# Kernel optimization log

Hardware: AMD Instinct MI355X
Metric: run time of the kernel (lower is better)

Reference implementation:

```python
import jax, jax.numpy as jnp
import numpy as np

QDEPTH = 20
WIDTH = HEIGHT = 28
PIXELS = WIDTH * HEIGHT          # 784
WIRES = 10                        # ceil(log2(784))
BATCH = 8192


def setup_inputs() -> dict:
    key = jax.random.key(0)
    k1, k2, k3, k4 = jax.random.split(key, 4)
    x = jax.random.normal(k1, (BATCH, 1, WIDTH, HEIGHT), jnp.float32)
    W = jax.random.normal(k2, (WIRES, PIXELS), jnp.float32) / np.sqrt(PIXELS)
    b = jax.random.normal(k3, (WIRES,), jnp.float32) * 0.01
    qweights = jax.random.normal(k4, (QDEPTH, WIRES, 3), jnp.float32) * 0.4
    return {"x": x, "W": W, "b": b, "qweights": qweights}


def _apply_1q(state, gate, wire):
    """Apply a single-qubit gate. state: (B,)+(2,)*WIRES; gate: (2,2) or (B,2,2)."""
    ax = 1 + wire
    s = jnp.moveaxis(state, ax, 1)
    shp = s.shape
    s = s.reshape(shp[0], 2, -1)
    if gate.ndim == 2:
        s = jnp.einsum('ij,bjr->bir', gate, s)
    else:
        s = jnp.einsum('bij,bjr->bir', gate, s)
    return jnp.moveaxis(s.reshape(shp), 1, ax)


def _cnot(state, c, t):
    """CNOT with control c, target t on state (B,)+(2,)*WIRES."""
    s = jnp.moveaxis(state, (1 + c, 1 + t), (1, 2))
    # when control==1, flip target axis
    s = jnp.concatenate([s[:, :1], jnp.flip(s[:, 1:2], axis=2)], axis=1)
    return jnp.moveaxis(s, (1, 2), (1 + c, 1 + t))


def _ry_batched(theta):
    """theta: (B,) -> (B,2,2) complex RY gates."""
    c = jnp.cos(theta / 2)
    s = jnp.sin(theta / 2)
    g = jnp.stack([jnp.stack([c, -s], -1), jnp.stack([s, c], -1)], -2)
    return g.astype(jnp.complex64)


def _rot(phi, theta, omega):
    """PennyLane Rot(phi,theta,omega) = RZ(omega) RY(theta) RZ(phi), scalars -> (2,2)."""
    c = jnp.cos(theta / 2)
    s = jnp.sin(theta / 2)
    m00 = jnp.exp(-0.5j * (phi + omega)) * c
    m01 = -jnp.exp(0.5j * (phi - omega)) * s
    m10 = jnp.exp(-0.5j * (phi - omega)) * s
    m11 = jnp.exp(0.5j * (phi + omega)) * c
    return jnp.stack([jnp.stack([m00, m01]), jnp.stack([m10, m11])]).astype(jnp.complex64)


def _forward(x, W, b, qweights):
    B = x.shape[0]
    feat = x.reshape(B, -1)                       # b 1 w h -> b (w h)
    angles = feat @ W.T + b                       # linear_down -> (B, WIRES)

    # |0...0> statevector, wire 0 most significant (PennyLane convention)
    state = jnp.zeros((B,) + (2,) * WIRES, jnp.complex64)
    state = state.at[(slice(None),) + (0,) * WIRES].set(1.0)

    # AngleEmbedding, rotation='Y'
    for w in range(WIRES):
        state = _apply_1q(state, _ry_batched(angles[:, w]), w)

    # StronglyEntanglingLayers: per-layer Rot on every wire, then CNOT ring
    for l in range(QDEPTH):
        for w in range(WIRES):
            state = _apply_1q(state, _rot(qweights[l, w, 0], qweights[l, w, 1], qweights[l, w, 2]), w)
        r = (l % (WIRES - 1)) + 1                 # default PennyLane ranges
        for w in range(WIRES):
            state = _cnot(state, w, (w + r) % WIRES)

    sv = state.reshape(B, -1)
    probs = sv.real ** 2 + sv.imag ** 2           # qml.probs over all wires
    out = jnp.clip(probs[:, :PIXELS] * PIXELS, 0.0, 1.0)
    return out.reshape(B, 1, WIDTH, HEIGHT)


def reference(x, W, b, qweights):
    return _forward(x, W, b, qweights)
```

## Files before the change

### kernel.cpp

```cpp
#include <hip/hip_runtime.h>
#include <hip/hip_bf16.h>
#include <stdint.h>


#define NWIRES  10
#define DIM     1024
#define NLAYERS 20
#define NGATES  200
#define NPASS   100
#define PIXELS  784
#define BATCH   8192

typedef _Float16 f16;
typedef _Float16 f16x8 __attribute__((ext_vector_type(8)));
typedef float    f32x4 __attribute__((ext_vector_type(4)));
typedef float    f32x2 __attribute__((ext_vector_type(2)));

typedef const __attribute__((address_space(1))) void* gas1_t;
typedef __attribute__((address_space(3))) void*       las3_t;

__device__ __forceinline__ void gload_lds16(const void* g, void* l) {
  __builtin_amdgcn_global_load_lds((gas1_t)g, (las3_t)l, 16, 0, 0);
}

__global__ __launch_bounds__(256) void k_prep(const float* __restrict__ qw,
                                              float* __restrict__ plan_mat,
                                              unsigned* __restrict__ plan_idx,
                                              unsigned* __restrict__ plan_final) {
  __shared__ float gm[NGATES][8];
  const int tid = threadIdx.x;

  if (tid < NGATES) {
    float phi = qw[tid * 3 + 0], th = qw[tid * 3 + 1], om = qw[tid * 3 + 2];
    float s, c, sa, ca, sb, cb;
    sincosf(0.5f * th, &s, &c);
    sincosf(0.5f * (phi + om), &sa, &ca);
    sincosf(0.5f * (phi - om), &sb, &cb);
    gm[tid][0] = ca * c;  gm[tid][1] = sa * c;
    gm[tid][2] = cb * s;  gm[tid][3] = sb * s;
    gm[tid][4] = -cb * s; gm[tid][5] = sb * s;
    gm[tid][6] = ca * c;  gm[tid][7] = -sa * c;
  }
  __syncthreads();

  if (tid == 0) {
    unsigned rowA[NWIRES], invc[NWIRES];
    for (int i = 0; i < NWIRES; i++) { rowA[i] = 1u << i; invc[i] = 1u << i; }
    for (int lrev = 0; lrev < NLAYERS; lrev++) {
      int l = NLAYERS - 1 - lrev;
      int r = (l % (NWIRES - 1)) + 1;
      for (int w = NWIRES - 1; w >= 0; w--) {
        int c = w, t = (w + r) % NWIRES;
        int pc = 9 - c, pt = 9 - t;
        rowA[pt] ^= rowA[pc];
        invc[pc] ^= invc[pt];
      }
      for (int s = 0; s < 5; s++) {
        int w1 = 2 * s, w2 = 2 * s + 1;
        int p1 = 9 - w1, p2 = 9 - w2;
        unsigned u1 = rowA[p1], u2 = rowA[p2];
        unsigned m1 = invc[p1], m2 = invc[p2];
        unsigned b1 = u1 & (0u - u1);
        if (u2 & b1) u2 ^= u1;
        unsigned b2 = u2 & (0u - u2);
        if (u1 & b2) u1 ^= u2;
        unsigned bLo = (b1 < b2) ? b1 : b2;
        unsigned bHi = (b1 < b2) ? b2 : b1;
        unsigned* P = plan_idx + (size_t)(lrev * 5 + s) * 8;
        P[0] = bLo; P[1] = bHi; P[2] = u1; P[3] = u2;
        P[4] = b1;  P[5] = b2;  P[6] = m1; P[7] = m2;
      }
    }
    for (int p = 0; p < NWIRES; p++) plan_final[p] = invc[p];
  } else if (tid >= 100 && tid < 200) {
    int t = tid - 100;
    int lrev = t / 5, s = t % 5;
    int l = NLAYERS - 1 - lrev;
    int g1 = l * NWIRES + 2 * s, g2 = g1 + 1;
    float* K = plan_mat + (size_t)t * 64;
#pragma unroll
    for (int r = 0; r < 4; r++) {
#pragma unroll
      for (int c = 0; c < 4; c++) {
        int r1 = r >> 1, c1 = c >> 1, r2 = r & 1, c2 = c & 1;
        float ar = gm[g1][(r1 * 2 + c1) * 2], ai = gm[g1][(r1 * 2 + c1) * 2 + 1];
        float br = gm[g2][(r2 * 2 + c2) * 2], bi = gm[g2][(r2 * 2 + c2) * 2 + 1];
        float kr = ar * br - ai * bi;
        float ki = ar * bi + ai * br;
        float* e = K + (r * 4 + c) * 4;
        e[0] = kr; e[1] = kr; e[2] = -ki; e[3] = ki;
      }
    }
  }
}

__global__ __launch_bounds__(256) void k_main(const float* __restrict__ plan_mat,
                                              const unsigned* __restrict__ plan_idx,
                                              const unsigned* __restrict__ plan_final,
                                              const float* __restrict__ x,
                                              const float* __restrict__ W,
                                              const float* __restrict__ bias,
                                              f16* __restrict__ E,
                                              f16* __restrict__ Bt) {
  __shared__ f32x2 st[DIM];
  __shared__ float part[4][NWIRES];
  __shared__ float csh[NWIRES][2];

  const int tid = threadIdx.x;

  if (blockIdx.x < PIXELS) {
    const int col = blockIdx.x;

    for (int i = tid; i < DIM; i += 256)
      st[i] = (f32x2){i == col ? 1.f : 0.f, 0.f};
    __syncthreads();

    for (int t = 0; t < NPASS; t++) {
      const unsigned* P = plan_idx + (size_t)t * 8;
      const unsigned bLo = P[0], bHi = P[1], u1 = P[2], u2 = P[3];
      const unsigned pb1 = P[4], pb2 = P[5], m1 = P[6], m2 = P[7];
      const f32x4* Kp = (const f32x4*)(plan_mat + (size_t)t * 64);

      unsigned q  = (unsigned)tid;
      unsigned xx = ((q & ~(bLo - 1u)) << 1) | (q & (bLo - 1u));
      unsigned j0 = ((xx & ~(bHi - 1u)) << 1) | (xx & (bHi - 1u));
      unsigned j  = j0 ^ ((__popc(u1 & j0) & 1) ? pb1 : 0u)
                       ^ ((__popc(u2 & j0) & 1) ? pb2 : 0u);

      f32x2 v0 = st[j];
      f32x2 v1 = st[j ^ m2];
      f32x2 v2 = st[j ^ m1];
      f32x2 v3 = st[j ^ m1 ^ m2];
      f32x2 w0 = {v0.y, v0.x}, w1 = {v1.y, v1.x};
      f32x2 w2 = {v2.y, v2.x}, w3 = {v3.y, v3.x};

      f32x2 r0 = {0.f, 0.f}, r1 = {0.f, 0.f}, r2 = {0.f, 0.f}, r3 = {0.f, 0.f};
#define CM(rr, e, vv, ww)                         \
      { f32x4 kk = Kp[e];                         \
        rr += (f32x2){kk.x, kk.y} * (vv);         \
        rr += (f32x2){kk.z, kk.w} * (ww); }
      CM(r0, 0, v0, w0)  CM(r0, 1, v1, w1)  CM(r0, 2, v2, w2)  CM(r0, 3, v3, w3)
      CM(r1, 4, v0, w0)  CM(r1, 5, v1, w1)  CM(r1, 6, v2, w2)  CM(r1, 7, v3, w3)
      CM(r2, 8, v0, w0)  CM(r2, 9, v1, w1)  CM(r2, 10, v2, w2) CM(r2, 11, v3, w3)
      CM(r3, 12, v0, w0) CM(r3, 13, v1, w1) CM(r3, 14, v2, w2) CM(r3, 15, v3, w3)
#undef CM

      st[j]           = r0;
      st[j ^ m2]      = r1;
      st[j ^ m1]      = r2;
      st[j ^ m1 ^ m2] = r3;
      __syncthreads();
    }

    unsigned invl[NWIRES];
#pragma unroll
    for (int p = 0; p < NWIRES; p++) invl[p] = plan_final[p];

    __align__(8) f16 re4[4], im4[4];
#pragma unroll
    for (int u = 0; u < 4; u++) {
      int i = tid * 4 + u;
      unsigned j = 0;
#pragma unroll
      for (int p = 0; p < NWIRES; p++)
        if ((i >> p) & 1) j ^= invl[p];
      f32x2 v = st[j];
      re4[u] = (f16)v.x;
      im4[u] = (f16)(-v.y);
    }
    *(uint2*)(&Bt[(size_t)(2 * col) * DIM + tid * 4])     = *(const uint2*)re4;
    *(uint2*)(&Bt[(size_t)(2 * col + 1) * DIM + tid * 4]) = *(const uint2*)im4;
    return;
  }

  const int b = blockIdx.x - PIXELS;
  const float* xr = x + (size_t)b * PIXELS;

  float acc[NWIRES];
#pragma unroll
  for (int w = 0; w < NWIRES; w++) acc[w] = 0.f;

  for (int k = tid; k < PIXELS; k += 256) {
    float xv = xr[k];
#pragma unroll
    for (int w = 0; w < NWIRES; w++) acc[w] = fmaf(xv, W[w * PIXELS + k], acc[w]);
  }

#pragma unroll
  for (int w = 0; w < NWIRES; w++) {
    float v = acc[w];
#pragma unroll
    for (int off = 32; off > 0; off >>= 1) v += __shfl_xor(v, off, 64);
    acc[w] = v;
  }

  const int wv = tid >> 6, ln = tid & 63;
  if (ln == 0) {
#pragma unroll
    for (int w = 0; w < NWIRES; w++) part[wv][w] = acc[w];
  }
  __syncthreads();
  if (tid < NWIRES) {
    float a = part[0][tid] + part[1][tid] + part[2][tid] + part[3][tid] + bias[tid];
    float s, c;
    sincosf(0.5f * a, &s, &c);
    csh[tid][0] = c;
    csh[tid][1] = s;
  }
  __syncthreads();

  __align__(8) f16 e4[4];
#pragma unroll
  for (int u = 0; u < 4; u++) {
    int i = tid * 4 + u;
    float pr = 1.f;
#pragma unroll
    for (int w = 0; w < NWIRES; w++) pr *= csh[w][(i >> (9 - w)) & 1];
    e4[u] = (f16)pr;
  }
  *(uint2*)(&E[(size_t)b * DIM + tid * 4]) = *(const uint2*)e4;
}

__device__ __forceinline__ void g_stage(const f16* __restrict__ g, f16* l,
                                        int tid, int row0, int kt) {
#pragma unroll
  for (int r = 0; r < 4; r++) {
    int u = r * 512 + tid;
    int row = u >> 3, c8 = u & 7;
    gload_lds16((const char*)g + (size_t)(row0 + row) * 2048 + kt * 128 + c8 * 16,
                (char*)l + (size_t)u * 16);
  }
}

__global__ __launch_bounds__(512, 2) void k_gemm(const f16* __restrict__ E,
                                                 const f16* __restrict__ Bt,
                                                 float* __restrict__ out) {
  __shared__ __align__(16) f16 As[2][256 * 64];
  __shared__ __align__(16) f16 Bs[2][256 * 64];

  const int tid = threadIdx.x;
  const int wid = tid >> 6, ln = tid & 63;
  const int wm = wid >> 2, wn = wid & 3;

  const int bid = blockIdx.x;
  const int swz = (bid & 7) * 28 + (bid >> 3);
  const int mt  = swz % 32, nt = swz / 32;
  const int m0  = mt * 256;
  const int n0  = nt * 256;

  f32x4 acc[8][4];
#pragma unroll
  for (int a = 0; a < 8; a++)
#pragma unroll
    for (int q = 0; q < 4; q++) acc[a][q] = (f32x4){0.f, 0.f, 0.f, 0.f};

#define COMPUTE(buf)                                                            \
  {                                                                             \
    _Pragma("unroll")                                                           \
    for (int kk = 0; kk < 2; kk++) {                                            \
      f16x8 af[8], bf[4];                                                       \
      _Pragma("unroll")                                                         \
      for (int mi = 0; mi < 8; mi++)                                            \
        af[mi] = *(const f16x8*)&As[buf][(wm * 128 + mi * 16 + (ln & 15)) * 64  \
                                         + kk * 32 + (ln >> 4) * 8];            \
      _Pragma("unroll")                                                         \
      for (int ni = 0; ni < 4; ni++)                                            \
        bf[ni] = *(const f16x8*)&Bs[buf][(wn * 64 + ni * 16 + (ln & 15)) * 64   \
                                         + kk * 32 + (ln >> 4) * 8];            \
      __builtin_amdgcn_s_setprio(1);                                            \
      _Pragma("unroll")                                                         \
      for (int mi = 0; mi < 8; mi++)                                            \
        _Pragma("unroll")                                                       \
        for (int ni = 0; ni < 4; ni++)                                          \
          acc[mi][ni] = __builtin_amdgcn_mfma_f32_16x16x32_f16(                 \
              af[mi], bf[ni], acc[mi][ni], 0, 0, 0);                            \
      __builtin_amdgcn_s_setprio(0);                                            \
    }                                                                           \
  }

  g_stage(E,  &As[0][0], tid, m0, 0);
  g_stage(Bt, &Bs[0][0], tid, n0, 0);
  __syncthreads();

  int cur = 0;
  for (int kt = 0; kt < 15; kt++) {
    g_stage(E,  &As[cur ^ 1][0], tid, m0, kt + 1);
    g_stage(Bt, &Bs[cur ^ 1][0], tid, n0, kt + 1);
    COMPUTE(cur);
    __syncthreads();
    cur ^= 1;
  }
  COMPUTE(cur);
#undef COMPUTE

#pragma unroll
  for (int mi = 0; mi < 8; mi++) {
#pragma unroll
    for (int ni = 0; ni < 4; ni++) {
      int n = n0 + wn * 64 + ni * 16 + (ln & 15);
      int p = n >> 1;
      bool even = (ln & 1) == 0;
#pragma unroll
      for (int r = 0; r < 4; r++) {
        float v = acc[mi][ni][r];
        float o = __shfl_xor(v, 1, 64);
        if (even && p < PIXELS) {
          int m = m0 + wm * 128 + mi * 16 + (ln >> 4) * 4 + r;
          float s2 = (v * v + o * o) * (float)PIXELS;
          out[(size_t)m * PIXELS + p] = fminf(fmaxf(s2, 0.f), 1.f);
        }
      }
    }
  }
}

extern "C" void kernel_launch(void* const* d_in, const int* in_sizes, int n_in,
                              void* d_out, int out_size, void* d_ws, size_t ws_size,
                              hipStream_t stream) {
  const float* x    = (const float*)d_in[0];
  const float* W    = (const float*)d_in[1];
  const float* bias = (const float*)d_in[2];
  const float* qw   = (const float*)d_in[3];
  float* out        = (float*)d_out;

  char* ws = (char*)d_ws;
  f16* E  = (f16*)(ws);
  f16* Bt = (f16*)(ws + (size_t)16 * 1024 * 1024);
  float*    plan_mat   = (float*)(ws + (size_t)20 * 1024 * 1024);
  unsigned* plan_idx   = (unsigned*)(ws + (size_t)20 * 1024 * 1024 + 65536);
  unsigned* plan_final = (unsigned*)(ws + (size_t)20 * 1024 * 1024 + 131072);

  k_prep<<<dim3(1), dim3(256), 0, stream>>>(qw, plan_mat, plan_idx, plan_final);
  k_main<<<dim3(PIXELS + BATCH), dim3(256), 0, stream>>>(plan_mat, plan_idx,
                                                         plan_final, x, W, bias,
                                                         E, Bt);
  k_gemm<<<dim3(224), dim3(512), 0, stream>>>(E, Bt, out);
}
```

Baseline: 143.1 us.

## XOR-swizzle LDS tiles and deepen GEMM prefetch with explicit vmcnt waits

The GEMM stores A and B tiles in LDS with an XOR swizzle on the 16-byte column chunk, keyed by row, and the fragment reads use the matching swizzled offsets. This is meant to remove LDS bank conflicts on the f16x8 reads. The main loop now keeps two tiles in flight, issuing the load for tile kt+2 right after computing tile kt, and replaces __syncthreads with explicit s_waitcnt vmcnt and s_barrier, plus sched_barrier to hold instruction order. This hides more global-load latency, but it relies on hand-counted outstanding loads and adds a third barrier per iteration.

```diff
diff --git a/kernel.cpp b/kernel.cpp
--- a/kernel.cpp
+++ b/kernel.cpp
@@ -225,8 +225,9 @@
                                         int tid, int row0, int kt) {
 #pragma unroll
   for (int r = 0; r < 4; r++) {
-    int u = r * 512 + tid;
-    int row = u >> 3, c8 = u & 7;
+    int u   = r * 512 + tid;
+    int row = u >> 3;
+    int c8  = (u & 7) ^ (row & 7);
     gload_lds16((const char*)g + (size_t)(row0 + row) * 2048 + kt * 128 + c8 * 16,
                 (char*)l + (size_t)u * 16);
   }
@@ -253,6 +254,8 @@
   for (int a = 0; a < 8; a++)
 #pragma unroll
     for (int q = 0; q < 4; q++) acc[a][q] = (f32x4){0.f, 0.f, 0.f, 0.f};
+
+#define SWZ_OFF(R, kk) ((R) * 64 + (((kk) * 4 + (ln >> 4)) ^ ((R) & 7)) * 8)
 
 #define COMPUTE(buf)                                                            \
   {                                                                             \
@@ -260,13 +263,15 @@
     for (int kk = 0; kk < 2; kk++) {                                            \
       f16x8 af[8], bf[4];                                                       \
       _Pragma("unroll")                                                         \
-      for (int mi = 0; mi < 8; mi++)                                            \
-        af[mi] = *(const f16x8*)&As[buf][(wm * 128 + mi * 16 + (ln & 15)) * 64  \
-                                         + kk * 32 + (ln >> 4) * 8];            \
+      for (int mi = 0; mi < 8; mi++) {                                          \
+        int Ra = wm * 128 + mi * 16 + (ln & 15);                                \
+        af[mi] = *(const f16x8*)&As[buf][SWZ_OFF(Ra, kk)];                      \
+      }                                                                         \
       _Pragma("unroll")                                                         \
-      for (int ni = 0; ni < 4; ni++)                                            \
-        bf[ni] = *(const f16x8*)&Bs[buf][(wn * 64 + ni * 16 + (ln & 15)) * 64   \
-                                         + kk * 32 + (ln >> 4) * 8];            \
+      for (int ni = 0; ni < 4; ni++) {                                          \
+        int Rb = wn * 64 + ni * 16 + (ln & 15);                                 \
+        bf[ni] = *(const f16x8*)&Bs[buf][SWZ_OFF(Rb, kk)];                      \
+      }                                                                         \
       __builtin_amdgcn_s_setprio(1);                                            \
       _Pragma("unroll")                                                         \
       for (int mi = 0; mi < 8; mi++)                                            \
@@ -280,18 +285,30 @@
 
   g_stage(E,  &As[0][0], tid, m0, 0);
   g_stage(Bt, &Bs[0][0], tid, n0, 0);
-  __syncthreads();
-
-  int cur = 0;
-  for (int kt = 0; kt < 15; kt++) {
-    g_stage(E,  &As[cur ^ 1][0], tid, m0, kt + 1);
-    g_stage(Bt, &Bs[cur ^ 1][0], tid, n0, kt + 1);
+  g_stage(E,  &As[1][0], tid, m0, 1);
+  g_stage(Bt, &Bs[1][0], tid, n0, 1);
+  asm volatile("s_waitcnt vmcnt(8)" ::: "memory");
+  __builtin_amdgcn_s_barrier();
+  __builtin_amdgcn_sched_barrier(0);
+
+  for (int kt = 0; kt < 16; kt++) {
+    const int cur = kt & 1;
     COMPUTE(cur);
-    __syncthreads();
-    cur ^= 1;
-  }
-  COMPUTE(cur);
+    __builtin_amdgcn_sched_barrier(0);
+    __builtin_amdgcn_s_barrier();
+    __builtin_amdgcn_sched_barrier(0);
+    if (kt + 2 < 16) {
+      g_stage(E,  &As[cur][0], tid, m0, kt + 2);
+      g_stage(Bt, &Bs[cur][0], tid, n0, kt + 2);
+      asm volatile("s_waitcnt vmcnt(8)" ::: "memory");
+    } else {
+      asm volatile("s_waitcnt vmcnt(0)" ::: "memory");
+    }
+    __builtin_amdgcn_s_barrier();
+    __builtin_amdgcn_sched_barrier(0);
+  }
 #undef COMPUTE
+#undef SWZ_OFF
 
 #pragma unroll
   for (int mi = 0; mi < 8; mi++) {
```

Result: faster. 134.8 us (-5.8%).

## Use 4-stage LDS pipeline with K=32 tiles and XOR-swizzled layout in GEMM

Applied to the files above, without the earlier changes.

The GEMM main loop moves from a double-buffered K=64 tile scheme to a 4-buffer ring of K=32 tiles. Global-to-LDS loads are issued three stages ahead, with explicit vmcnt waits and raw barriers in place of __syncthreads. The LDS layout gets an XOR swizzle on the 16-byte column chunks to cut bank conflicts, and the fragment offsets are precomputed. This aims to hide global load latency better, at the cost of more barriers per unit of K and hand-tuned waitcnt values that are easy to get wrong.

```diff
diff --git a/kernel.cpp b/kernel.cpp
--- a/kernel.cpp
+++ b/kernel.cpp
@@ -221,22 +221,11 @@
   *(uint2*)(&E[(size_t)b * DIM + tid * 4]) = *(const uint2*)e4;
 }
 
-__device__ __forceinline__ void g_stage(const f16* __restrict__ g, f16* l,
-                                        int tid, int row0, int kt) {
-#pragma unroll
-  for (int r = 0; r < 4; r++) {
-    int u = r * 512 + tid;
-    int row = u >> 3, c8 = u & 7;
-    gload_lds16((const char*)g + (size_t)(row0 + row) * 2048 + kt * 128 + c8 * 16,
-                (char*)l + (size_t)u * 16);
-  }
-}
-
 __global__ __launch_bounds__(512, 2) void k_gemm(const f16* __restrict__ E,
                                                  const f16* __restrict__ Bt,
                                                  float* __restrict__ out) {
-  __shared__ __align__(16) f16 As[2][256 * 64];
-  __shared__ __align__(16) f16 Bs[2][256 * 64];
+  __shared__ __align__(16) f16 As[4][256 * 32];
+  __shared__ __align__(16) f16 Bs[4][256 * 32];
 
   const int tid = threadIdx.x;
   const int wid = tid >> 6, ln = tid & 63;
@@ -254,44 +243,69 @@
 #pragma unroll
     for (int q = 0; q < 4; q++) acc[a][q] = (f32x4){0.f, 0.f, 0.f, 0.f};
 
-#define COMPUTE(buf)                                                            \
-  {                                                                             \
-    _Pragma("unroll")                                                           \
-    for (int kk = 0; kk < 2; kk++) {                                            \
-      f16x8 af[8], bf[4];                                                       \
-      _Pragma("unroll")                                                         \
-      for (int mi = 0; mi < 8; mi++)                                            \
-        af[mi] = *(const f16x8*)&As[buf][(wm * 128 + mi * 16 + (ln & 15)) * 64  \
-                                         + kk * 32 + (ln >> 4) * 8];            \
-      _Pragma("unroll")                                                         \
-      for (int ni = 0; ni < 4; ni++)                                            \
-        bf[ni] = *(const f16x8*)&Bs[buf][(wn * 64 + ni * 16 + (ln & 15)) * 64   \
-                                         + kk * 32 + (ln >> 4) * 8];            \
-      __builtin_amdgcn_s_setprio(1);                                            \
-      _Pragma("unroll")                                                         \
-      for (int mi = 0; mi < 8; mi++)                                            \
-        _Pragma("unroll")                                                       \
-        for (int ni = 0; ni < 4; ni++)                                          \
-          acc[mi][ni] = __builtin_amdgcn_mfma_f32_16x16x32_f16(                 \
-              af[mi], bf[ni], acc[mi][ni], 0, 0, 0);                            \
-      __builtin_amdgcn_s_setprio(0);                                            \
-    }                                                                           \
-  }
-
-  g_stage(E,  &As[0][0], tid, m0, 0);
-  g_stage(Bt, &Bs[0][0], tid, n0, 0);
-  __syncthreads();
-
-  int cur = 0;
-  for (int kt = 0; kt < 15; kt++) {
-    g_stage(E,  &As[cur ^ 1][0], tid, m0, kt + 1);
-    g_stage(Bt, &Bs[cur ^ 1][0], tid, n0, kt + 1);
-    COMPUTE(cur);
-    __syncthreads();
-    cur ^= 1;
-  }
-  COMPUTE(cur);
-#undef COMPUTE
+  int offA[8], offB[4];
+#pragma unroll
+  for (int mi = 0; mi < 8; mi++) {
+    int Ra = wm * 128 + mi * 16 + (ln & 15);
+    offA[mi] = Ra * 32 + (((ln >> 4) ^ ((Ra >> 1) & 3)) * 8);
+  }
+#pragma unroll
+  for (int ni = 0; ni < 4; ni++) {
+    int Rb = wn * 64 + ni * 16 + (ln & 15);
+    offB[ni] = Rb * 32 + (((ln >> 4) ^ ((Rb >> 1) & 3)) * 8);
+  }
+
+  auto stage = [&](int t) {
+    const int sb = t & 3;
+#pragma unroll
+    for (int r = 0; r < 2; r++) {
+      int u   = r * 512 + tid;
+      int row = u >> 2;
+      int c16 = (u & 3) ^ ((row >> 1) & 3);
+      gload_lds16((const char*)E + (size_t)(m0 + row) * 2048 + t * 64 + c16 * 16,
+                  (char*)&As[sb][0] + (size_t)u * 16);
+    }
+#pragma unroll
+    for (int r = 0; r < 2; r++) {
+      int u   = r * 512 + tid;
+      int row = u >> 2;
+      int c16 = (u & 3) ^ ((row >> 1) & 3);
+      gload_lds16((const char*)Bt + (size_t)(n0 + row) * 2048 + t * 64 + c16 * 16,
+                  (char*)&Bs[sb][0] + (size_t)u * 16);
+    }
+  };
+
+  stage(0);
+  stage(1);
+  stage(2);
+  asm volatile("s_waitcnt vmcnt(8)" ::: "memory");
+  __builtin_amdgcn_s_barrier();
+
+#pragma unroll 4
+  for (int k = 0; k < 32; k++) {
+    const int buf = k & 3;
+    f16x8 af[8], bf[4];
+#pragma unroll
+    for (int mi = 0; mi < 8; mi++) af[mi] = *(const f16x8*)&As[buf][offA[mi]];
+#pragma unroll
+    for (int ni = 0; ni < 4; ni++) bf[ni] = *(const f16x8*)&Bs[buf][offB[ni]];
+
+    if (k < 29) stage(k + 3);
+
+    __builtin_amdgcn_s_setprio(1);
+#pragma unroll
+    for (int mi = 0; mi < 8; mi++)
+#pragma unroll
+      for (int ni = 0; ni < 4; ni++)
+        acc[mi][ni] = __builtin_amdgcn_mfma_f32_16x16x32_f16(
+            af[mi], bf[ni], acc[mi][ni], 0, 0, 0);
+    __builtin_amdgcn_s_setprio(0);
+
+    if (k < 29)       { asm volatile("s_waitcnt vmcnt(8)" ::: "memory"); }
+    else if (k == 29) { asm volatile("s_waitcnt vmcnt(4)" ::: "memory"); }
+    else if (k == 30) { asm volatile("s_waitcnt vmcnt(0)" ::: "memory"); }
+    __builtin_amdgcn_s_barrier();
+  }
 
 #pragma unroll
   for (int mi = 0; mi < 8; mi++) {
```

New measurement: 130.5 us. 1.1x faster.
